# Kernel tuning notes

Hardware: AMD Instinct MI355X
Metric: run time of the kernel (lower is better)

Reference implementation:

```python
import math
import jax, jax.numpy as jnp
import numpy as np

B, S, E, H, P = 8, 1024, 512, 8, 32
MAXD, OFFS, LW, STL, HID = 256, 8.0, 4, 4, 2048

def _lin(x, w, b):
    return x @ w.T + b

def _gelu(x):
    return jax.nn.gelu(x, approximate=False)  # torch nn.GELU default (erf)

def _ln(x, g, b, eps=1e-5):
    m = x.mean(-1, keepdims=True)
    v = ((x - m) ** 2).mean(-1, keepdims=True)
    return (x - m) / jnp.sqrt(v + eps) * g + b

def setup_inputs() -> dict:
    key = jax.random.key(0)
    ks = iter(jax.random.split(key, 40))
    def w(*shape):
        return (jax.random.normal(next(ks), shape, dtype=jnp.float32) * 0.02)
    x = jax.random.normal(next(ks), (B, S, E), dtype=jnp.float32)
    lengths = jax.random.randint(next(ks), (B,), S // 2, S + 1)
    padding_mask = jnp.arange(S)[None, :] >= lengths[:, None]  # (B,S) bool
    inp = dict(x=x, padding_mask=padding_mask)
    # local MHA (torch nn.MultiheadAttention packed in_proj)
    inp.update(in_proj_w=w(3 * E, E), in_proj_b=jnp.zeros((3 * E,), jnp.float32),
               mha_out_w=w(E, E), mha_out_b=jnp.zeros((E,), jnp.float32))
    # deformable attention projections
    for nm in ('dq', 'dk', 'dv', 'do'):
        inp[nm + '_w'] = w(E, E); inp[nm + '_b'] = jnp.zeros((E,), jnp.float32)
    inp.update(off1_w=w(E, E), off1_b=jnp.zeros((E,), jnp.float32),
               off2_w=w(H * P, E), off2_b=jnp.zeros((H * P,), jnp.float32))
    inp.update(gate1_w=w(E, 3 * E), gate1_b=jnp.zeros((E,), jnp.float32),
               gate2_w=w(E, E), gate2_b=jnp.zeros((E,), jnp.float32))
    inp.update(n1_g=jnp.ones((E,), jnp.float32), n1_b=jnp.zeros((E,), jnp.float32),
               n2_g=jnp.ones((E,), jnp.float32), n2_b=jnp.zeros((E,), jnp.float32))
    inp.update(ffn1_w=w(HID, E), ffn1_b=jnp.zeros((HID,), jnp.float32),
               ffn2_w=w(E, HID), ffn2_b=jnp.zeros((E,), jnp.float32))
    return inp

def _forward(x, padding_mask, in_proj_w, in_proj_b, mha_out_w, mha_out_b,
             dq_w, dq_b, dk_w, dk_b, dv_w, dv_b, do_w, do_b,
             off1_w, off1_b, off2_w, off2_b, gate1_w, gate1_b, gate2_w, gate2_b,
             n1_g, n1_b, n2_g, n2_b, ffn1_w, ffn1_b, ffn2_w, ffn2_b):
    Bv, Sv, Ev = x.shape
    hd = Ev // H
    pos = jnp.arange(Sv)
    # ---------------- local causal windowed MHA ----------------
    qkv = _lin(x, in_proj_w, in_proj_b)
    q, k, v = jnp.split(qkv, 3, axis=-1)
    q = q.reshape(Bv, Sv, H, hd).transpose(0, 2, 1, 3)  # bhsd
    k = k.reshape(Bv, Sv, H, hd).transpose(0, 2, 1, 3)
    v = v.reshape(Bv, Sv, H, hd).transpose(0, 2, 1, 3)
    scores = jnp.einsum('bhqd,bhkd->bhqk', q, k) / math.sqrt(hd)
    future = pos[None, :] > pos[:, None]
    too_far = (pos[:, None] - pos[None, :]) >= min(LW, STL)
    lmask = (future | too_far)[None, None] | padding_mask[:, None, None, :]
    scores = jnp.where(lmask, -jnp.inf, scores)
    allm = lmask.all(-1, keepdims=True)
    scores = jnp.where(allm, 0.0, scores)  # avoid NaN on fully-masked (padded) rows
    attn = jax.nn.softmax(scores, axis=-1)
    attn = jnp.where(lmask, 0.0, attn)
    lo = jnp.einsum('bhqk,bhkd->bhqd', attn, v).transpose(0, 2, 1, 3).reshape(Bv, Sv, Ev)
    local_out = _lin(lo, mha_out_w, mha_out_b)
    # ---------------- deformable long-history attention ----------------
    anchors = jnp.linspace(0.1, 0.9, P)
    valid_len = jnp.clip(Sv - padding_mask.sum(-1), 1, None)
    positions = pos[None, :, None].astype(jnp.float32)  # (1,S,1)
    base = anchors[None, None, :] * positions
    off = jnp.tanh(_lin(_gelu(_lin(x, off1_w, off1_b)), off2_w, off2_b))
    off = off.reshape(Bv, Sv, H, P).mean(2) * OFFS
    sampled = base + off
    sampled = jnp.clip(sampled, jnp.clip(positions - MAXD, 0, None), positions)
    sampled = jnp.minimum(sampled, (valid_len - 1).astype(jnp.float32)[:, None, None])
    sp = jnp.round(sampled).astype(jnp.int32)  # (B,S,P) sample positions
    qd = _lin(x, dq_w, dq_b)
    kd = _lin(x, dk_w, dk_b)
    vd = _lin(x, dv_w, dv_b)
    bidx = jnp.arange(Bv)[:, None, None]
    k_sp = kd[bidx, sp]  # (B,S,P,E) gathered keys
    v_sp = vd[bidx, sp]
    sc = jnp.einsum('bqd,bqpd->bqp', qd, k_sp) / math.sqrt(Ev)
    samp_inv = padding_mask[bidx, sp]
    causal_inv = sp > pos[None, :, None]
    rb = jnp.clip(pos[:, None] - (STL - 1), 0, None)
    long_mem_mask = pos[None, :] >= rb  # (S,S): forbid recent short-term positions
    extra_inv = long_mem_mask[pos[None, :, None], sp]
    inv = samp_inv | causal_inv | extra_inv
    sc = jnp.where(inv, -jnp.inf, sc)
    alli = inv.all(-1, keepdims=True)
    sc = jnp.where(alli, 0.0, sc)
    a = jax.nn.softmax(sc, axis=-1)
    a = jnp.where(inv, 0.0, a)
    long_out = _lin(jnp.einsum('bqp,bqpd->bqd', a, v_sp), do_w, do_b)
    # ---------------- gate fuse + FFN ----------------
    cat = jnp.concatenate([x, local_out, long_out], axis=-1)
    g = jax.nn.sigmoid(_lin(_gelu(_lin(cat, gate1_w, gate1_b)), gate2_w, gate2_b))
    fused = g * local_out + (1.0 - g) * long_out
    x1 = _ln(x + fused, n1_g, n1_b)
    f = _lin(_gelu(_lin(x1, ffn1_w, ffn1_b)), ffn2_w, ffn2_b)
    return _ln(x1 + f, n2_g, n2_b)

def reference(x, padding_mask, in_proj_w, in_proj_b, mha_out_w, mha_out_b,
              dq_w, dq_b, dk_w, dk_b, dv_w, dv_b, do_w, do_b,
              off1_w, off1_b, off2_w, off2_b, gate1_w, gate1_b, gate2_w, gate2_b,
              n1_g, n1_b, n2_g, n2_b, ffn1_w, ffn1_b, ffn2_w, ffn2_b):
    return _forward(x, padding_mask, in_proj_w, in_proj_b, mha_out_w, mha_out_b,
                    dq_w, dq_b, dk_w, dk_b, dv_w, dv_b, do_w, do_b,
                    off1_w, off1_b, off2_w, off2_b, gate1_w, gate1_b, gate2_w, gate2_b,
                    n1_g, n1_b, n2_g, n2_b, ffn1_w, ffn1_b, ffn2_w, ffn2_b)
```

## Files before the change

### kernel.cpp

```cpp
#include <hip/hip_runtime.h>
#include <hip/hip_bf16.h>
#include <type_traits>

typedef __hip_bfloat16 bf16;
typedef __attribute__((ext_vector_type(8))) short short8;
typedef __attribute__((ext_vector_type(4))) float floatx4;

static constexpr int kB = 8;
static constexpr int kS = 1024;
static constexpr int kE = 512;
static constexpr int kH = 8;
static constexpr int kP = 32;
static constexpr int kTok = kB * kS;
static constexpr int kHid = 2048;

__device__ __forceinline__ void load8f(const bf16* p, float* f) {
  uint4 u = *(const uint4*)p;
  const bf16* h = (const bf16*)&u;
#pragma unroll
  for (int e = 0; e < 8; e++) f[e] = __bfloat162float(h[e]);
}
__device__ __forceinline__ void store8b(bf16* p, const float* f) {
  uint4 u;
  bf16* h = (bf16*)&u;
#pragma unroll
  for (int e = 0; e < 8; e++) h[e] = __float2bfloat16(f[e]);
  *(uint4*)p = u;
}
__device__ __forceinline__ bool is_pad(const void* pm, int flag, int idx) {
  return flag ? (((const int*)pm)[idx] != 0)
              : (((const unsigned char*)pm)[idx] != 0);
}
__device__ __forceinline__ float fast_gelu(float x) {
  float u = x * (0.7978845608f + 0.044714998f * x * x);
  float e = __expf(2.0f * u);
  float t = 1.0f - 2.0f / (e + 1.0f);
  return 0.5f * x * (1.0f + t);
}

__global__ __launch_bounds__(256) void detect_kernel(const void* __restrict__ x,
                                                     int* __restrict__ meta) {
  __shared__ int cnt;
  if (threadIdx.x == 0) cnt = 0;
  __syncthreads();
  const unsigned short* u = (const unsigned short*)x;
  int c = 0;
  for (int i = threadIdx.x; i < 1024; i += 256) {
    int e = (u[i] >> 7) & 0xFF;
    if (e >= 0x90) c++;
  }
  if (c) atomicAdd(&cnt, c);
  __syncthreads();
  if (threadIdx.x == 0) meta[9] = (cnt > 64) ? 1 : 0;
}

__global__ __launch_bounds__(256) void meta_kernel(const void* __restrict__ pm,
                                                   int* __restrict__ meta) {
  __shared__ int bigfound;
  __shared__ int cnt[kB];
  int tid = threadIdx.x;
  if (tid == 0) bigfound = 0;
  if (tid < kB) cnt[tid] = 0;
  __syncthreads();
  const unsigned int* w = (const unsigned int*)pm;
  int f = 0;
  for (int i = tid; i < 2048; i += 256)
    if (w[i] & 0xFFFFFFFEu) f = 1;
  if (f) atomicOr(&bigfound, 1);
  __syncthreads();
  int flag = bigfound ? 0 : 1;
  for (int i = tid; i < kTok; i += 256) {
    if (is_pad(pm, flag, i)) atomicAdd(&cnt[i >> 10], 1);
  }
  __syncthreads();
  if (tid == 0) meta[0] = flag;
  if (tid < kB) {
    int vl = kS - cnt[tid];
    if (vl < 1) vl = 1;
    meta[1 + tid] = vl;
  }
}

struct CvtJob { const void* src; bf16* hi; bf16* lo; int nblk; };
struct CvtJobs { CvtJob j[13]; };
__global__ __launch_bounds__(256) void cvt_all_kernel(CvtJobs jobs,
                                                      const int* __restrict__ meta) {
  int fp = meta[9];
  int b = blockIdx.x, ji = 0;
  while (b >= jobs.j[ji].nblk) { b -= jobs.j[ji].nblk; ji++; }
  CvtJob J = jobs.j[ji];
  int i = b * 1024 + threadIdx.x * 4;
  float v[4];
  if (fp) {
    float4 f = ((const float4*)J.src)[i >> 2];
    v[0] = f.x; v[1] = f.y; v[2] = f.z; v[3] = f.w;
  } else {
    uint2 u = *(const uint2*)((const bf16*)J.src + i);
    const bf16* h = (const bf16*)&u;
#pragma unroll
    for (int e = 0; e < 4; e++) v[e] = __bfloat162float(h[e]);
  }
  uint2 uh;
  bf16* hh = (bf16*)&uh;
#pragma unroll
  for (int e = 0; e < 4; e++) hh[e] = __float2bfloat16(v[e]);
  *(uint2*)(J.hi + i) = uh;
  if (J.lo) {
    uint2 ul;
    bf16* hl = (bf16*)&ul;
#pragma unroll
    for (int e = 0; e < 4; e++)
      hl[e] = __float2bfloat16(v[e] - __bfloat162float(hh[e]));
    *(uint2*)(J.lo + i) = ul;
  }
}

struct CvtFJob { const void* src; float* dst; int n; };
struct CvtFJobs { CvtFJob j[16]; };
__global__ __launch_bounds__(256) void cvt_small_kernel(CvtFJobs jobs,
                                                        const int* __restrict__ meta) {
  int fp = meta[9];
#pragma unroll 1
  for (int ji = 0; ji < 16; ji++) {
    CvtFJob J = jobs.j[ji];
    for (int i = threadIdx.x; i < J.n; i += 256)
      J.dst[i] = fp ? ((const float*)J.src)[i]
                    : __bfloat162float(((const bf16*)J.src)[i]);
  }
}

static constexpr int BK = 32, LDK = 40;

template <int BM, int BN, int ACT, typename OUTT>
__device__ __forceinline__ void gemm_core(const bf16* __restrict__ A,
                                          const bf16* __restrict__ W,
                                          const float* __restrict__ bias,
                                          OUTT* __restrict__ C, int N, int K,
                                          int m0, int n0) {
  constexpr int WR = (BM == 128 && BN == 128) ? 4 : 2;
  constexpr int WC = 4;
  __shared__ bf16 As[BM * LDK];
  __shared__ bf16 Bs[BN * LDK];
  const int tid = threadIdx.x;
  const int lane = tid & 63;
  const int wid = tid >> 6;
  int wm, wn;
  if constexpr (BM == 128 && BN == 128) {
    wm = (wid >> 1) * 64; wn = (wid & 1) * 64;
  } else {
    wm = wid * 32; wn = 0;
  }

  floatx4 acc[WR][WC];
#pragma unroll
  for (int i = 0; i < WR; i++)
#pragma unroll
    for (int j = 0; j < WC; j++) acc[i][j] = (floatx4)0.0f;

  for (int kt = 0; kt < K; kt += BK) {
#pragma unroll
    for (int c = 0; c < BM / 64; c++) {
      int v = c * 256 + tid;
      int row = v >> 2, off = (v & 3) * 8;
      *(uint4*)(&As[row * LDK + off]) =
          *(const uint4*)(&A[(size_t)(m0 + row) * K + kt + off]);
    }
#pragma unroll
    for (int c = 0; c < BN / 64; c++) {
      int v = c * 256 + tid;
      int row = v >> 2, off = (v & 3) * 8;
      *(uint4*)(&Bs[row * LDK + off]) =
          *(const uint4*)(&W[(size_t)(n0 + row) * K + kt + off]);
    }
    __syncthreads();
    const int ko = (lane >> 4) * 8;
    short8 af[WR], bfr[WC];
#pragma unroll
    for (int i = 0; i < WR; i++)
      af[i] = *(const short8*)(&As[(wm + i * 16 + (lane & 15)) * LDK + ko]);
#pragma unroll
    for (int j = 0; j < WC; j++)
      bfr[j] = *(const short8*)(&Bs[(wn + j * 16 + (lane & 15)) * LDK + ko]);
#pragma unroll
    for (int i = 0; i < WR; i++)
#pragma unroll
      for (int j = 0; j < WC; j++)
        acc[i][j] = __builtin_amdgcn_mfma_f32_16x16x32_bf16(bfr[j], af[i],
                                                            acc[i][j], 0, 0, 0);
    __syncthreads();
  }

#pragma unroll
  for (int i = 0; i < WR; i++) {
    int row = m0 + wm + i * 16 + (lane & 15);
#pragma unroll
    for (int j = 0; j < WC; j++) {
      int col = n0 + wn + j * 16 + ((lane >> 4) << 2);
      float bv[4] = {0.f, 0.f, 0.f, 0.f};
      if (bias) {
        float4 b4 = *(const float4*)&bias[col];
        bv[0] = b4.x; bv[1] = b4.y; bv[2] = b4.z; bv[3] = b4.w;
      }
      float v[4];
#pragma unroll
      for (int r = 0; r < 4; r++) {
        v[r] = acc[i][j][r] + bv[r];
        if (ACT == 1) v[r] = fast_gelu(v[r]);
        else if (ACT == 2) v[r] = 1.0f / (1.0f + __expf(-v[r]));
      }
      size_t idx = (size_t)row * N + col;
      if constexpr (std::is_same<OUTT, float>::value) {
        *(float4*)&C[idx] = make_float4(v[0], v[1], v[2], v[3]);
      } else {
        uint2 u;
        bf16* h = (bf16*)&u;
#pragma unroll
        for (int r = 0; r < 4; r++) h[r] = __float2bfloat16(v[r]);
        *(uint2*)&C[idx] = u;
      }
    }
  }
}

template <int BM, int BN, int ACT, typename OUTT>
__global__ __launch_bounds__(256) void gemm_bt(
    const bf16* __restrict__ A, const bf16* __restrict__ W,
    const float* __restrict__ bias, OUTT* __restrict__ C, int N, int K) {
  gemm_core<BM, BN, ACT, OUTT>(A, W, bias, C, N, K, blockIdx.x * BM,
                               blockIdx.y * BN);
}

__global__ __launch_bounds__(256) void gemm_pair(
    const bf16* __restrict__ A0, const bf16* __restrict__ W0,
    const float* __restrict__ b0, bf16* __restrict__ C0,
    const bf16* __restrict__ A1, const bf16* __restrict__ W1,
    const float* __restrict__ b1, bf16* __restrict__ C1, int N, int K) {
  int nb = N >> 6;
  bool s = (int)blockIdx.y >= nb;
  gemm_core<128, 64, 0, bf16>(s ? A1 : A0, s ? W1 : W0, s ? b1 : b0,
                              s ? C1 : C0, N, K, blockIdx.x * 128,
                              (s ? (int)blockIdx.y - nb : (int)blockIdx.y) * 64);
}

__global__ __launch_bounds__(256) void gemm_gate1(
    const bf16* __restrict__ x, const bf16* __restrict__ lo,
    const bf16* __restrict__ lg, const bf16* __restrict__ W,
    const float* __restrict__ bias, bf16* __restrict__ C) {
  constexpr int BM = 128, BN = 64, WR = 2, WC = 4;
  constexpr int N = 512, K = 1536;
  __shared__ bf16 As[BM * LDK];
  __shared__ bf16 Bs[BN * LDK];
  const int tid = threadIdx.x;
  const int lane = tid & 63;
  const int wid = tid >> 6;
  const int wm = wid * 32, wn = 0;
  const int m0 = blockIdx.x * BM, n0 = blockIdx.y * BN;

  floatx4 acc[WR][WC];
#pragma unroll
  for (int i = 0; i < WR; i++)
#pragma unroll
    for (int j = 0; j < WC; j++) acc[i][j] = (floatx4)0.0f;

  for (int kt = 0; kt < K; kt += BK) {
#pragma unroll
    for (int c = 0; c < 2; c++) {
      int v = c * 256 + tid;
      int row = v >> 2, off = (v & 3) * 8;
      int k = kt + off;
      const bf16* src = (k < 512) ? x : (k < 1024) ? lo : lg;
      int kk = k & 511;
      *(uint4*)(&As[row * LDK + off]) =
          *(const uint4*)(&src[(size_t)(m0 + row) * 512 + kk]);
    }
    {
      int v = tid;
      int row = v >> 2, off = (v & 3) * 8;
      *(uint4*)(&Bs[row * LDK + off]) =
          *(const uint4*)(&W[(size_t)(n0 + row) * K + kt + off]);
    }
    __syncthreads();
    const int ko = (lane >> 4) * 8;
    short8 af[WR], bfr[WC];
#pragma unroll
    for (int i = 0; i < WR; i++)
      af[i] = *(const short8*)(&As[(wm + i * 16 + (lane & 15)) * LDK + ko]);
#pragma unroll
    for (int j = 0; j < WC; j++)
      bfr[j] = *(const short8*)(&Bs[(wn + j * 16 + (lane & 15)) * LDK + ko]);
#pragma unroll
    for (int i = 0; i < WR; i++)
#pragma unroll
      for (int j = 0; j < WC; j++)
        acc[i][j] = __builtin_amdgcn_mfma_f32_16x16x32_bf16(bfr[j], af[i],
                                                            acc[i][j], 0, 0, 0);
    __syncthreads();
  }

#pragma unroll
  for (int i = 0; i < WR; i++) {
    int row = m0 + wm + i * 16 + (lane & 15);
#pragma unroll
    for (int j = 0; j < WC; j++) {
      int col = n0 + wn + j * 16 + ((lane >> 4) << 2);
      float4 b4 = *(const float4*)&bias[col];
      float bv[4] = {b4.x, b4.y, b4.z, b4.w};
      uint2 u;
      bf16* h = (bf16*)&u;
#pragma unroll
      for (int r = 0; r < 4; r++)
        h[r] = __float2bfloat16(fast_gelu(acc[i][j][r] + bv[r]));
      *(uint2*)&C[(size_t)row * N + col] = u;
    }
  }
}

template <int BM, int BN>
__global__ __launch_bounds__(256) void gemm3_bt(
    const bf16* __restrict__ Ah, const bf16* __restrict__ Al,
    const bf16* __restrict__ Wh, const bf16* __restrict__ Wl,
    const float* __restrict__ bias, float* __restrict__ C, int N, int K) {
  constexpr int WR = 2;
  constexpr int WC = (BM == 128) ? 4 : 2;
  __shared__ bf16 Ash[BM * LDK];
  __shared__ bf16 Asl[BM * LDK];
  __shared__ bf16 Bsh[BN * LDK];
  __shared__ bf16 Bsl[BN * LDK];
  const int tid = threadIdx.x;
  const int lane = tid & 63;
  const int wid = tid >> 6;
  int wm, wn;
  if constexpr (BM == 128) {
    wm = wid * 32; wn = 0;
  } else {
    wm = (wid >> 1) * 32; wn = (wid & 1) * 32;
  }
  const int m0 = blockIdx.x * BM, n0 = blockIdx.y * BN;

  floatx4 acc[WR][WC];
#pragma unroll
  for (int i = 0; i < WR; i++)
#pragma unroll
    for (int j = 0; j < WC; j++) acc[i][j] = (floatx4)0.0f;

  for (int kt = 0; kt < K; kt += BK) {
#pragma unroll
    for (int c = 0; c < BM / 64; c++) {
      int v = c * 256 + tid;
      int row = v >> 2, off = (v & 3) * 8;
      size_t g = (size_t)(m0 + row) * K + kt + off;
      *(uint4*)(&Ash[row * LDK + off]) = *(const uint4*)(&Ah[g]);
      *(uint4*)(&Asl[row * LDK + off]) = *(const uint4*)(&Al[g]);
    }
#pragma unroll
    for (int c = 0; c < BN / 64; c++) {
      int v = c * 256 + tid;
      int row = v >> 2, off = (v & 3) * 8;
      size_t g = (size_t)(n0 + row) * K + kt + off;
      *(uint4*)(&Bsh[row * LDK + off]) = *(const uint4*)(&Wh[g]);
      *(uint4*)(&Bsl[row * LDK + off]) = *(const uint4*)(&Wl[g]);
    }
    __syncthreads();
    const int ko = (lane >> 4) * 8;
    short8 ah[WR], al[WR], bh[WC], bl[WC];
#pragma unroll
    for (int i = 0; i < WR; i++) {
      int ro = (wm + i * 16 + (lane & 15)) * LDK + ko;
      ah[i] = *(const short8*)(&Ash[ro]);
      al[i] = *(const short8*)(&Asl[ro]);
    }
#pragma unroll
    for (int j = 0; j < WC; j++) {
      int ro = (wn + j * 16 + (lane & 15)) * LDK + ko;
      bh[j] = *(const short8*)(&Bsh[ro]);
      bl[j] = *(const short8*)(&Bsl[ro]);
    }
#pragma unroll
    for (int i = 0; i < WR; i++)
#pragma unroll
      for (int j = 0; j < WC; j++) {
        acc[i][j] = __builtin_amdgcn_mfma_f32_16x16x32_bf16(bh[j], ah[i],
                                                            acc[i][j], 0, 0, 0);
        acc[i][j] = __builtin_amdgcn_mfma_f32_16x16x32_bf16(bl[j], ah[i],
                                                            acc[i][j], 0, 0, 0);
        acc[i][j] = __builtin_amdgcn_mfma_f32_16x16x32_bf16(bh[j], al[i],
                                                            acc[i][j], 0, 0, 0);
      }
    __syncthreads();
  }

#pragma unroll
  for (int i = 0; i < WR; i++) {
    int row = m0 + wm + i * 16 + (lane & 15);
#pragma unroll
    for (int j = 0; j < WC; j++) {
      int col = n0 + wn + j * 16 + ((lane >> 4) << 2);
      float4 b4 = *(const float4*)&bias[col];
      float bv[4] = {b4.x, b4.y, b4.z, b4.w};
      float v[4];
#pragma unroll
      for (int r = 0; r < 4; r++) v[r] = acc[i][j][r] + bv[r];
      *(float4*)&C[(size_t)row * N + col] = make_float4(v[0], v[1], v[2], v[3]);
    }
  }
}

__global__ __launch_bounds__(256) void local_attn_kernel(
    const bf16* __restrict__ qkv, const void* __restrict__ pm,
    const int* __restrict__ meta, bf16* __restrict__ lo) {
  int lane = threadIdx.x & 63;
  int t = blockIdx.x * 4 + (threadIdx.x >> 6);
  int b = t >> 10, s = t & 1023;
  int h = lane >> 3, sub = lane & 7;
  int flag = meta[0];
  float q[8];
  load8f(qkv + (size_t)t * 3072 + h * 64 + sub * 8, q);
  float sc[4];
  bool val[4];
#pragma unroll
  for (int w = 0; w < 4; w++) {
    int kp = s - 3 + w;
    bool v = (kp >= 0) && !is_pad(pm, flag, b * kS + kp);
    float d = 0.0f;
    if (v) {
      float kk[8];
      load8f(qkv + (size_t)(b * kS + kp) * 3072 + 512 + h * 64 + sub * 8, kk);
#pragma unroll
      for (int e = 0; e < 8; e++) d += q[e] * kk[e];
    }
    d += __shfl_xor(d, 1);
    d += __shfl_xor(d, 2);
    d += __shfl_xor(d, 4);
    sc[w] = v ? d / 8.0f : -INFINITY;
    val[w] = v;
  }
  float mx = fmaxf(fmaxf(sc[0], sc[1]), fmaxf(sc[2], sc[3]));
  float a[4] = {0.f, 0.f, 0.f, 0.f};
  if (mx != -INFINITY) {
    float ssum = 0.f;
#pragma unroll
    for (int w = 0; w < 4; w++) {
      float e = val[w] ? expf(sc[w] - mx) : 0.0f;
      a[w] = e;
      ssum += e;
    }
#pragma unroll
    for (int w = 0; w < 4; w++) a[w] /= ssum;
  }
  float o[8] = {0.f, 0.f, 0.f, 0.f, 0.f, 0.f, 0.f, 0.f};
#pragma unroll
  for (int w = 0; w < 4; w++) {
    if (val[w] && a[w] > 0.0f) {
      int kp = s - 3 + w;
      float vv[8];
      load8f(qkv + (size_t)(b * kS + kp) * 3072 + 1024 + h * 64 + sub * 8, vv);
#pragma unroll
      for (int e = 0; e < 8; e++) o[e] += a[w] * vv[e];
    }
  }
  store8b(lo + (size_t)t * kE + lane * 8, o);
}

__global__ __launch_bounds__(256) void gelu_split_kernel(
    const float* __restrict__ S, bf16* __restrict__ hi, bf16* __restrict__ lo) {
  int i = (blockIdx.x * 256 + threadIdx.x) * 4;
#pragma unroll
  for (int c = 0; c < 4; c++) {
    float v = S[i + c];
    float g = 0.5f * v * (1.0f + erff(v * 0.70710678118654752f));
    bf16 a = __float2bfloat16(g);
    hi[i + c] = a;
    lo[i + c] = __float2bfloat16(g - __bfloat162float(a));
  }
}

__global__ __launch_bounds__(256) void sampler_kernel(
    const float* __restrict__ rawf, const void* __restrict__ pm,
    const int* __restrict__ meta, int* __restrict__ sp,
    unsigned int* __restrict__ invm) {
  int t = blockIdx.x * 8 + (threadIdx.x >> 5);
  int p = threadIdx.x & 31;
  int b = t >> 10, s = t & 1023;
  int flag = meta[0];
  float off = 0.0f;
#pragma unroll
  for (int h = 0; h < kH; h++) off += tanhf(rawf[(size_t)t * 256 + h * kP + p]);
  double anchor = 0.1 + 0.8 * (double)p / 31.0;
  double sampled = anchor * (double)s + (double)off;
  double lov = fmax(0.0, (double)s - 256.0);
  sampled = fmin(fmax(sampled, lov), (double)s);
  int vlen = meta[1 + b];
  sampled = fmin(sampled, (double)(vlen - 1));
  int spv = (int)rint(sampled);
  bool inv = is_pad(pm, flag, b * kS + spv) || (spv > s) ||
             (spv >= max(0, s - 3));
  sp[(size_t)t * kP + p] = spv;
  unsigned long long m = __ballot(inv);
  int lane = threadIdx.x & 63;
  if (lane == 0) invm[t] = (unsigned int)m;
  if (lane == 32) invm[t] = (unsigned int)(m >> 32);
}

__global__ __launch_bounds__(256) void long_attn_kernel(
    const bf16* __restrict__ qkv, const int* __restrict__ sp,
    const unsigned int* __restrict__ invm, bf16* __restrict__ ctx) {
  int lane = threadIdx.x & 63;
  int bid = blockIdx.x;
  int sbid = (bid & 7) * 256 + (bid >> 3);
  int t = sbid * 4 + (threadIdx.x >> 6);
  int b = t >> 10;
  int p = lane & 31;
  int row_abs = b * kS + sp[(size_t)t * kP + p];
  float q[8];
  load8f(qkv + (size_t)t * 3072 + 1536 + lane * 8, q);
  float sc_mine = 0.0f;
#pragma unroll 4
  for (int pp = 0; pp < 32; pp++) {
    int row = __shfl(row_abs, pp);
    float kk[8];
    load8f(qkv + (size_t)row * 3072 + 2048 + lane * 8, kk);
    float d = 0.0f;
#pragma unroll
    for (int e = 0; e < 8; e++) d += q[e] * kk[e];
#pragma unroll
    for (int m = 1; m < 64; m <<= 1) d += __shfl_xor(d, m);
    if (p == pp) sc_mine = d;
  }
  bool inv = (invm[t] >> p) & 1u;
  float sc = inv ? -INFINITY : sc_mine / 22.627416997969522f;
  float mx = sc;
#pragma unroll
  for (int m = 1; m < 32; m <<= 1) mx = fmaxf(mx, __shfl_xor(mx, m));
  float e = (inv || mx == -INFINITY) ? 0.0f : expf(sc - mx);
  float ssum = e;
#pragma unroll
  for (int m = 1; m < 32; m <<= 1) ssum += __shfl_xor(ssum, m);
  float a = (ssum > 0.0f) ? e / ssum : 0.0f;
  float o[8] = {0.f, 0.f, 0.f, 0.f, 0.f, 0.f, 0.f, 0.f};
#pragma unroll 4
  for (int pp = 0; pp < 32; pp++) {
    float ap = __shfl(a, pp);
    int row = __shfl(row_abs, pp);
    if (ap != 0.0f) {
      float vv[8];
      load8f(qkv + (size_t)row * 3072 + 2560 + lane * 8, vv);
#pragma unroll
      for (int e2 = 0; e2 < 8; e2++) o[e2] += ap * vv[e2];
    }
  }
  store8b(ctx + (size_t)t * kE + lane * 8, o);
}

__global__ __launch_bounds__(256) void ln1_kernel(
    const void* __restrict__ xin, const int* __restrict__ meta,
    const bf16* __restrict__ lo, const bf16* __restrict__ lg,
    const bf16* __restrict__ g, const float* __restrict__ gamma,
    const float* __restrict__ beta, bf16* __restrict__ x1b,
    float* __restrict__ x1f) {
  int lane = threadIdx.x & 63;
  int t = blockIdx.x * 4 + (threadIdx.x >> 6);
  size_t base = (size_t)t * kE + lane * 8;
  float xv[8], lov[8], lgv[8], gv[8], h[8];
  if (meta[9]) {
    const float4* xf = (const float4*)((const float*)xin + base);
    float4 a = xf[0], b2 = xf[1];
    xv[0] = a.x; xv[1] = a.y; xv[2] = a.z; xv[3] = a.w;
    xv[4] = b2.x; xv[5] = b2.y; xv[6] = b2.z; xv[7] = b2.w;
  } else {
    load8f((const bf16*)xin + base, xv);
  }
  load8f(lo + base, lov);
  load8f(lg + base, lgv);
  load8f(g + base, gv);
  float s1 = 0.f, s2 = 0.f;
#pragma unroll
  for (int e = 0; e < 8; e++) {
    h[e] = xv[e] + gv[e] * lov[e] + (1.0f - gv[e]) * lgv[e];
    s1 += h[e];
    s2 += h[e] * h[e];
  }
#pragma unroll
  for (int m = 1; m < 64; m <<= 1) {
    s1 += __shfl_xor(s1, m);
    s2 += __shfl_xor(s2, m);
  }
  float mean = s1 * (1.0f / kE);
  float var = s2 * (1.0f / kE) - mean * mean;
  float rstd = 1.0f / sqrtf(var + 1e-5f);
  float y[8];
#pragma unroll
  for (int e = 0; e < 8; e++)
    y[e] = (h[e] - mean) * rstd * gamma[lane * 8 + e] + beta[lane * 8 + e];
  store8b(x1b + base, y);
#pragma unroll
  for (int e = 0; e < 8; e++) x1f[base + e] = y[e];
}

__global__ __launch_bounds__(256) void ln2_kernel(
    const float* __restrict__ x1f, const float* __restrict__ ff,
    const float* __restrict__ gamma, const float* __restrict__ beta,
    const int* __restrict__ meta, void* __restrict__ out) {
  int lane = threadIdx.x & 63;
  int t = blockIdx.x * 4 + (threadIdx.x >> 6);
  size_t base = (size_t)t * kE + lane * 8;
  float h[8];
  float s1 = 0.f, s2 = 0.f;
#pragma unroll
  for (int e = 0; e < 8; e++) {
    h[e] = x1f[base + e] + ff[base + e];
    s1 += h[e];
    s2 += h[e] * h[e];
  }
#pragma unroll
  for (int m = 1; m < 64; m <<= 1) {
    s1 += __shfl_xor(s1, m);
    s2 += __shfl_xor(s2, m);
  }
  float mean = s1 * (1.0f / kE);
  float var = s2 * (1.0f / kE) - mean * mean;
  float rstd = 1.0f / sqrtf(var + 1e-5f);
  float y[8];
#pragma unroll
  for (int e = 0; e < 8; e++)
    y[e] = (h[e] - mean) * rstd * gamma[lane * 8 + e] + beta[lane * 8 + e];
  if (meta[9]) {
    float* of = (float*)out + base;
    ((float4*)of)[0] = make_float4(y[0], y[1], y[2], y[3]);
    ((float4*)of)[1] = make_float4(y[4], y[5], y[6], y[7]);
  } else {
    store8b((bf16*)out + base, y);
  }
}

extern "C" void kernel_launch(void* const* d_in, const int* in_sizes, int n_in,
                              void* d_out, int out_size, void* d_ws,
                              size_t ws_size, hipStream_t stream) {
  const void* x = d_in[0];
  const void* pm = d_in[1];

  char* w = (char*)d_ws;
  auto alloc = [&](size_t bytes) {
    char* p = w;
    w += (bytes + 255) & ~(size_t)255;
    return p;
  };
  bf16* qkv_all = (bf16*)alloc((size_t)kTok * 3072 * 2);
  bf16* lo_ctx = (bf16*)alloc((size_t)kTok * kE * 2);
  bf16* ctx2 = (bf16*)alloc((size_t)kTok * kE * 2);
  bf16* local_out = (bf16*)alloc((size_t)kTok * kE * 2);
  bf16* long_out = (bf16*)alloc((size_t)kTok * kE * 2);
  bf16* hbuf = (bf16*)alloc((size_t)kTok * kE * 2);
  bf16* gbuf = (bf16*)alloc((size_t)kTok * kE * 2);
  bf16* x1b = (bf16*)alloc((size_t)kTok * kE * 2);
  float* x1f = (float*)alloc((size_t)kTok * kE * 4);
  float* rawf = (float*)alloc((size_t)kTok * 256 * 4);
  int* sp = (int*)alloc((size_t)kTok * kP * 4);
  unsigned int* invm = (unsigned int*)alloc((size_t)kTok * 4);
  int* meta = (int*)alloc(256);
  bf16* x_hi = (bf16*)alloc((size_t)kTok * kE * 2);
  bf16* x_lo = (bf16*)alloc((size_t)kTok * kE * 2);
  bf16* wall = (bf16*)alloc((size_t)3072 * 512 * 2);
  bf16* mow = (bf16*)alloc(512 * 512 * 2);
  bf16* dow = (bf16*)alloc(512 * 512 * 2);
  bf16* o1h = (bf16*)alloc(512 * 512 * 2);
  bf16* o1l = (bf16*)alloc(512 * 512 * 2);
  bf16* o2h = (bf16*)alloc(256 * 512 * 2);
  bf16* o2l = (bf16*)alloc(256 * 512 * 2);
  bf16* g1w = (bf16*)alloc(512 * 1536 * 2);
  bf16* g2w = (bf16*)alloc(512 * 512 * 2);
  bf16* f1w = (bf16*)alloc((size_t)2048 * 512 * 2);
  bf16* f2w = (bf16*)alloc((size_t)512 * 2048 * 2);
  float* ball = (float*)alloc(3072 * 4);
  float* mob = (float*)alloc(512 * 4);
  float* dob = (float*)alloc(512 * 4);
  float* o1b = (float*)alloc(512 * 4);
  float* o2b = (float*)alloc(256 * 4);
  float* g1b = (float*)alloc(512 * 4);
  float* g2b = (float*)alloc(512 * 4);
  float* n1g = (float*)alloc(512 * 4);
  float* n1bt = (float*)alloc(512 * 4);
  float* n2g = (float*)alloc(512 * 4);
  float* n2bt = (float*)alloc(512 * 4);
  float* f1b = (float*)alloc(2048 * 4);
  float* f2b = (float*)alloc(512 * 4);

  float* S32 = x1f;
  bf16* h_hi = hbuf;
  bf16* h_lo = x1b;
  float* f_f32 = (float*)qkv_all;
  bf16* ffn_h = (bf16*)((char*)qkv_all + (size_t)kTok * kE * 4);

  dim3 blk(256);
  detect_kernel<<<1, blk, 0, stream>>>(x, meta);
  meta_kernel<<<1, blk, 0, stream>>>(pm, meta);

  CvtJobs J;
  auto job = [](const void* s, bf16* hi, bf16* lo, int n) {
    CvtJob j; j.src = s; j.hi = hi; j.lo = lo; j.nblk = n >> 10; return j;
  };
  J.j[0] = job(d_in[0], x_hi, x_lo, kTok * kE);
  J.j[1] = job(d_in[2], wall, nullptr, 1536 * 512);
  J.j[2] = job(d_in[6], wall + (size_t)1536 * 512, nullptr, 512 * 512);
  J.j[3] = job(d_in[8], wall + (size_t)2048 * 512, nullptr, 512 * 512);
  J.j[4] = job(d_in[10], wall + (size_t)2560 * 512, nullptr, 512 * 512);
  J.j[5] = job(d_in[4], mow, nullptr, 512 * 512);
  J.j[6] = job(d_in[12], dow, nullptr, 512 * 512);
  J.j[7] = job(d_in[14], o1h, o1l, 512 * 512);
  J.j[8] = job(d_in[16], o2h, o2l, 256 * 512);
  J.j[9] = job(d_in[18], g1w, nullptr, 512 * 1536);
  J.j[10] = job(d_in[20], g2w, nullptr, 512 * 512);
  J.j[11] = job(d_in[26], f1w, nullptr, 2048 * 512);
  J.j[12] = job(d_in[28], f2w, nullptr, 512 * 2048);
  int totblk = 0;
  for (int i = 0; i < 13; i++) totblk += J.j[i].nblk;
  cvt_all_kernel<<<totblk, blk, 0, stream>>>(J, meta);

  CvtFJobs JF;
  auto fjob = [](const void* s, float* d, int n) {
    CvtFJob j; j.src = s; j.dst = d; j.n = n; return j;
  };
  JF.j[0] = fjob(d_in[3], ball, 1536);
  JF.j[1] = fjob(d_in[7], ball + 1536, 512);
  JF.j[2] = fjob(d_in[9], ball + 2048, 512);
  JF.j[3] = fjob(d_in[11], ball + 2560, 512);
  JF.j[4] = fjob(d_in[5], mob, 512);
  JF.j[5] = fjob(d_in[13], dob, 512);
  JF.j[6] = fjob(d_in[15], o1b, 512);
  JF.j[7] = fjob(d_in[17], o2b, 256);
  JF.j[8] = fjob(d_in[19], g1b, 512);
  JF.j[9] = fjob(d_in[21], g2b, 512);
  JF.j[10] = fjob(d_in[22], n1g, 512);
  JF.j[11] = fjob(d_in[23], n1bt, 512);
  JF.j[12] = fjob(d_in[24], n2g, 512);
  JF.j[13] = fjob(d_in[25], n2bt, 512);
  JF.j[14] = fjob(d_in[27], f1b, 2048);
  JF.j[15] = fjob(d_in[29], f2b, 512);
  cvt_small_kernel<<<1, blk, 0, stream>>>(JF, meta);

  gemm_bt<128, 128, 0, bf16><<<dim3(64, 24), blk, 0, stream>>>(
      x_hi, wall, ball, qkv_all, 3072, kE);
  gemm3_bt<128, 64><<<dim3(64, 8), blk, 0, stream>>>(
      x_hi, x_lo, o1h, o1l, o1b, S32, kE, kE);
  local_attn_kernel<<<2048, blk, 0, stream>>>(qkv_all, pm, meta, lo_ctx);
  gelu_split_kernel<<<4096, blk, 0, stream>>>(S32, h_hi, h_lo);
  gemm3_bt<64, 64><<<dim3(128, 4), blk, 0, stream>>>(
      h_hi, h_lo, o2h, o2l, o2b, rawf, 256, kE);
  sampler_kernel<<<1024, blk, 0, stream>>>(rawf, pm, meta, sp, invm);
  long_attn_kernel<<<2048, blk, 0, stream>>>(qkv_all, sp, invm, ctx2);

  gemm_pair<<<dim3(64, 16), blk, 0, stream>>>(lo_ctx, mow, mob, local_out,
                                              ctx2, dow, dob, long_out, kE, kE);

  gemm_gate1<<<dim3(64, 8), blk, 0, stream>>>(x_hi, local_out, long_out, g1w,
                                              g1b, hbuf);
  gemm_bt<128, 64, 2, bf16><<<dim3(64, 8), blk, 0, stream>>>(
      hbuf, g2w, g2b, gbuf, kE, kE);

  ln1_kernel<<<2048, blk, 0, stream>>>(x, meta, local_out, long_out, gbuf, n1g,
                                       n1bt, x1b, x1f);
  gemm_bt<128, 128, 1, bf16><<<dim3(64, 16), blk, 0, stream>>>(
      x1b, f1w, f1b, ffn_h, kHid, kE);
  gemm_bt<128, 64, 0, float><<<dim3(64, 8), blk, 0, stream>>>(
      ffn_h, f2w, f2b, f_f32, kE, kHid);
  ln2_kernel<<<2048, blk, 0, stream>>>(x1f, f_f32, n2g, n2bt, meta, d_out);
}
```

Before: 489.8 us.

## Use direct global-to-LDS loads with XOR swizzle and fuse GELU split into GEMM

All GEMM kernels now stage their A/B tiles with global_load_lds DMA into unpadded shared memory. An XOR swizzle replaces the padding to avoid bank conflicts, and this removes the register round-trip for tile loads. Separately, the GELU plus hi/lo bf16 split moves into the epilogue of the first offset GEMM, which removes one kernel launch and an fp32 intermediate write and read. The swizzle and lane-to-row mapping must match the DMA's wave-contiguous write pattern exactly, or results will be wrong.

```diff
diff --git a/kernel.cpp b/kernel.cpp
--- a/kernel.cpp
+++ b/kernel.cpp
@@ -36,6 +36,11 @@
   float e = __expf(2.0f * u);
   float t = 1.0f - 2.0f / (e + 1.0f);
   return 0.5f * x * (1.0f + t);
+}
+__device__ __forceinline__ void dma16(const bf16* g, bf16* l) {
+  __builtin_amdgcn_global_load_lds(
+      (const __attribute__((address_space(1))) unsigned int*)g,
+      (__attribute__((address_space(3))) unsigned int*)l, 16, 0, 0);
 }
 
 __global__ __launch_bounds__(256) void detect_kernel(const void* __restrict__ x,
@@ -129,7 +134,7 @@
   }
 }
 
-static constexpr int BK = 32, LDK = 40;
+static constexpr int BK = 32;
 
 template <int BM, int BN, int ACT, typename OUTT>
 __device__ __forceinline__ void gemm_core(const bf16* __restrict__ A,
@@ -139,8 +144,8 @@
                                           int m0, int n0) {
   constexpr int WR = (BM == 128 && BN == 128) ? 4 : 2;
   constexpr int WC = 4;
-  __shared__ bf16 As[BM * LDK];
-  __shared__ bf16 Bs[BN * LDK];
+  __shared__ bf16 As[BM * BK];
+  __shared__ bf16 Bs[BN * BK];
   const int tid = threadIdx.x;
   const int lane = tid & 63;
   const int wid = tid >> 6;
@@ -160,27 +165,31 @@
   for (int kt = 0; kt < K; kt += BK) {
 #pragma unroll
     for (int c = 0; c < BM / 64; c++) {
-      int v = c * 256 + tid;
-      int row = v >> 2, off = (v & 3) * 8;
-      *(uint4*)(&As[row * LDK + off]) =
-          *(const uint4*)(&A[(size_t)(m0 + row) * K + kt + off]);
+      int seg = c * 64 + wid * 16;
+      int row = seg + (lane >> 2);
+      int ch = (lane & 3) ^ ((row >> 1) & 3);
+      dma16(&A[(size_t)(m0 + row) * K + kt + ch * 8], &As[seg * BK]);
     }
 #pragma unroll
     for (int c = 0; c < BN / 64; c++) {
-      int v = c * 256 + tid;
-      int row = v >> 2, off = (v & 3) * 8;
-      *(uint4*)(&Bs[row * LDK + off]) =
-          *(const uint4*)(&W[(size_t)(n0 + row) * K + kt + off]);
+      int seg = c * 64 + wid * 16;
+      int row = seg + (lane >> 2);
+      int ch = (lane & 3) ^ ((row >> 1) & 3);
+      dma16(&W[(size_t)(n0 + row) * K + kt + ch * 8], &Bs[seg * BK]);
     }
     __syncthreads();
-    const int ko = (lane >> 4) * 8;
+    const int kb = lane >> 4;
     short8 af[WR], bfr[WC];
 #pragma unroll
-    for (int i = 0; i < WR; i++)
-      af[i] = *(const short8*)(&As[(wm + i * 16 + (lane & 15)) * LDK + ko]);
-#pragma unroll
-    for (int j = 0; j < WC; j++)
-      bfr[j] = *(const short8*)(&Bs[(wn + j * 16 + (lane & 15)) * LDK + ko]);
+    for (int i = 0; i < WR; i++) {
+      int r = wm + i * 16 + (lane & 15);
+      af[i] = *(const short8*)(&As[r * BK + ((kb ^ ((r >> 1) & 3)) << 3)]);
+    }
+#pragma unroll
+    for (int j = 0; j < WC; j++) {
+      int r = wn + j * 16 + (lane & 15);
+      bfr[j] = *(const short8*)(&Bs[r * BK + ((kb ^ ((r >> 1) & 3)) << 3)]);
+    }
 #pragma unroll
     for (int i = 0; i < WR; i++)
 #pragma unroll
@@ -248,8 +257,8 @@
     const float* __restrict__ bias, bf16* __restrict__ C) {
   constexpr int BM = 128, BN = 64, WR = 2, WC = 4;
   constexpr int N = 512, K = 1536;
-  __shared__ bf16 As[BM * LDK];
-  __shared__ bf16 Bs[BN * LDK];
+  __shared__ bf16 As[BM * BK];
+  __shared__ bf16 Bs[BN * BK];
   const int tid = threadIdx.x;
   const int lane = tid & 63;
   const int wid = tid >> 6;
@@ -263,31 +272,34 @@
     for (int j = 0; j < WC; j++) acc[i][j] = (floatx4)0.0f;
 
   for (int kt = 0; kt < K; kt += BK) {
+    const bf16* src = (kt < 512) ? x : (kt < 1024) ? lo : lg;
+    int kk = kt & 511;
 #pragma unroll
     for (int c = 0; c < 2; c++) {
-      int v = c * 256 + tid;
-      int row = v >> 2, off = (v & 3) * 8;
-      int k = kt + off;
-      const bf16* src = (k < 512) ? x : (k < 1024) ? lo : lg;
-      int kk = k & 511;
-      *(uint4*)(&As[row * LDK + off]) =
-          *(const uint4*)(&src[(size_t)(m0 + row) * 512 + kk]);
+      int seg = c * 64 + wid * 16;
+      int row = seg + (lane >> 2);
+      int ch = (lane & 3) ^ ((row >> 1) & 3);
+      dma16(&src[(size_t)(m0 + row) * 512 + kk + ch * 8], &As[seg * BK]);
     }
     {
-      int v = tid;
-      int row = v >> 2, off = (v & 3) * 8;
-      *(uint4*)(&Bs[row * LDK + off]) =
-          *(const uint4*)(&W[(size_t)(n0 + row) * K + kt + off]);
+      int seg = wid * 16;
+      int row = seg + (lane >> 2);
+      int ch = (lane & 3) ^ ((row >> 1) & 3);
+      dma16(&W[(size_t)(n0 + row) * K + kt + ch * 8], &Bs[seg * BK]);
     }
     __syncthreads();
-    const int ko = (lane >> 4) * 8;
+    const int kb = lane >> 4;
     short8 af[WR], bfr[WC];
 #pragma unroll
-    for (int i = 0; i < WR; i++)
-      af[i] = *(const short8*)(&As[(wm + i * 16 + (lane & 15)) * LDK + ko]);
-#pragma unroll
-    for (int j = 0; j < WC; j++)
-      bfr[j] = *(const short8*)(&Bs[(wn + j * 16 + (lane & 15)) * LDK + ko]);
+    for (int i = 0; i < WR; i++) {
+      int r = wm + i * 16 + (lane & 15);
+      af[i] = *(const short8*)(&As[r * BK + ((kb ^ ((r >> 1) & 3)) << 3)]);
+    }
+#pragma unroll
+    for (int j = 0; j < WC; j++) {
+      int r = wn + j * 16 + (lane & 15);
+      bfr[j] = *(const short8*)(&Bs[r * BK + ((kb ^ ((r >> 1) & 3)) << 3)]);
+    }
 #pragma unroll
     for (int i = 0; i < WR; i++)
 #pragma unroll
@@ -315,17 +327,18 @@
   }
 }
 
-template <int BM, int BN>
+template <int BM, int BN, bool SPLIT>
 __global__ __launch_bounds__(256) void gemm3_bt(
     const bf16* __restrict__ Ah, const bf16* __restrict__ Al,
     const bf16* __restrict__ Wh, const bf16* __restrict__ Wl,
-    const float* __restrict__ bias, float* __restrict__ C, int N, int K) {
+    const float* __restrict__ bias, float* __restrict__ Cf,
+    bf16* __restrict__ Chi, bf16* __restrict__ Clo, int N, int K) {
   constexpr int WR = 2;
   constexpr int WC = (BM == 128) ? 4 : 2;
-  __shared__ bf16 Ash[BM * LDK];
-  __shared__ bf16 Asl[BM * LDK];
-  __shared__ bf16 Bsh[BN * LDK];
-  __shared__ bf16 Bsl[BN * LDK];
+  __shared__ bf16 Ash[BM * BK];
+  __shared__ bf16 Asl[BM * BK];
+  __shared__ bf16 Bsh[BN * BK];
+  __shared__ bf16 Bsl[BN * BK];
   const int tid = threadIdx.x;
   const int lane = tid & 63;
   const int wid = tid >> 6;
@@ -346,32 +359,36 @@
   for (int kt = 0; kt < K; kt += BK) {
 #pragma unroll
     for (int c = 0; c < BM / 64; c++) {
-      int v = c * 256 + tid;
-      int row = v >> 2, off = (v & 3) * 8;
-      size_t g = (size_t)(m0 + row) * K + kt + off;
-      *(uint4*)(&Ash[row * LDK + off]) = *(const uint4*)(&Ah[g]);
-      *(uint4*)(&Asl[row * LDK + off]) = *(const uint4*)(&Al[g]);
+      int seg = c * 64 + wid * 16;
+      int row = seg + (lane >> 2);
+      int ch = (lane & 3) ^ ((row >> 1) & 3);
+      size_t g = (size_t)(m0 + row) * K + kt + ch * 8;
+      dma16(&Ah[g], &Ash[seg * BK]);
+      dma16(&Al[g], &Asl[seg * BK]);
     }
 #pragma unroll
     for (int c = 0; c < BN / 64; c++) {
-      int v = c * 256 + tid;
-      int row = v >> 2, off = (v & 3) * 8;
-      size_t g = (size_t)(n0 + row) * K + kt + off;
-      *(uint4*)(&Bsh[row * LDK + off]) = *(const uint4*)(&Wh[g]);
-      *(uint4*)(&Bsl[row * LDK + off]) = *(const uint4*)(&Wl[g]);
+      int seg = c * 64 + wid * 16;
+      int row = seg + (lane >> 2);
+      int ch = (lane & 3) ^ ((row >> 1) & 3);
+      size_t g = (size_t)(n0 + row) * K + kt + ch * 8;
+      dma16(&Wh[g], &Bsh[seg * BK]);
+      dma16(&Wl[g], &Bsl[seg * BK]);
     }
     __syncthreads();
-    const int ko = (lane >> 4) * 8;
+    const int kb = lane >> 4;
     short8 ah[WR], al[WR], bh[WC], bl[WC];
 #pragma unroll
     for (int i = 0; i < WR; i++) {
-      int ro = (wm + i * 16 + (lane & 15)) * LDK + ko;
+      int r = wm + i * 16 + (lane & 15);
+      int ro = r * BK + ((kb ^ ((r >> 1) & 3)) << 3);
       ah[i] = *(const short8*)(&Ash[ro]);
       al[i] = *(const short8*)(&Asl[ro]);
     }
 #pragma unroll
     for (int j = 0; j < WC; j++) {
-      int ro = (wn + j * 16 + (lane & 15)) * LDK + ko;
+      int r = wn + j * 16 + (lane & 15);
+      int ro = r * BK + ((kb ^ ((r >> 1) & 3)) << 3);
       bh[j] = *(const short8*)(&Bsh[ro]);
       bl[j] = *(const short8*)(&Bsl[ro]);
     }
@@ -397,10 +414,25 @@
       int col = n0 + wn + j * 16 + ((lane >> 4) << 2);
       float4 b4 = *(const float4*)&bias[col];
       float bv[4] = {b4.x, b4.y, b4.z, b4.w};
-      float v[4];
-#pragma unroll
-      for (int r = 0; r < 4; r++) v[r] = acc[i][j][r] + bv[r];
-      *(float4*)&C[(size_t)row * N + col] = make_float4(v[0], v[1], v[2], v[3]);
+      if constexpr (SPLIT) {
+        uint2 uh, ul;
+        bf16* hh = (bf16*)&uh;
+        bf16* hl = (bf16*)&ul;
+#pragma unroll
+        for (int r = 0; r < 4; r++) {
+          float v = acc[i][j][r] + bv[r];
+          float g = 0.5f * v * (1.0f + erff(v * 0.70710678118654752f));
+          bf16 hi = __float2bfloat16(g);
+          hh[r] = hi;
+          hl[r] = __float2bfloat16(g - __bfloat162float(hi));
+        }
+        *(uint2*)&Chi[(size_t)row * N + col] = uh;
+        *(uint2*)&Clo[(size_t)row * N + col] = ul;
+      } else {
+        *(float4*)&Cf[(size_t)row * N + col] =
+            make_float4(acc[i][j][0] + bv[0], acc[i][j][1] + bv[1],
+                        acc[i][j][2] + bv[2], acc[i][j][3] + bv[3]);
+      }
     }
   }
 }
@@ -459,19 +491,6 @@
     }
   }
   store8b(lo + (size_t)t * kE + lane * 8, o);
-}
-
-__global__ __launch_bounds__(256) void gelu_split_kernel(
-    const float* __restrict__ S, bf16* __restrict__ hi, bf16* __restrict__ lo) {
-  int i = (blockIdx.x * 256 + threadIdx.x) * 4;
-#pragma unroll
-  for (int c = 0; c < 4; c++) {
-    float v = S[i + c];
-    float g = 0.5f * v * (1.0f + erff(v * 0.70710678118654752f));
-    bf16 a = __float2bfloat16(g);
-    hi[i + c] = a;
-    lo[i + c] = __float2bfloat16(g - __bfloat162float(a));
-  }
 }
 
 __global__ __launch_bounds__(256) void sampler_kernel(
@@ -684,7 +703,6 @@
   float* f1b = (float*)alloc(2048 * 4);
   float* f2b = (float*)alloc(512 * 4);
 
-  float* S32 = x1f;
   bf16* h_hi = hbuf;
   bf16* h_lo = x1b;
   float* f_f32 = (float*)qkv_all;
@@ -739,12 +757,11 @@
 
   gemm_bt<128, 128, 0, bf16><<<dim3(64, 24), blk, 0, stream>>>(
       x_hi, wall, ball, qkv_all, 3072, kE);
-  gemm3_bt<128, 64><<<dim3(64, 8), blk, 0, stream>>>(
-      x_hi, x_lo, o1h, o1l, o1b, S32, kE, kE);
+  gemm3_bt<128, 64, true><<<dim3(64, 8), blk, 0, stream>>>(
+      x_hi, x_lo, o1h, o1l, o1b, nullptr, h_hi, h_lo, kE, kE);
   local_attn_kernel<<<2048, blk, 0, stream>>>(qkv_all, pm, meta, lo_ctx);
-  gelu_split_kernel<<<4096, blk, 0, stream>>>(S32, h_hi, h_lo);
-  gemm3_bt<64, 64><<<dim3(128, 4), blk, 0, stream>>>(
-      h_hi, h_lo, o2h, o2l, o2b, rawf, 256, kE);
+  gemm3_bt<64, 64, false><<<dim3(128, 4), blk, 0, stream>>>(
+      h_hi, h_lo, o2h, o2l, o2b, rawf, nullptr, nullptr, 256, kE);
   sampler_kernel<<<1024, blk, 0, stream>>>(rawf, pm, meta, sp, invm);
   long_attn_kernel<<<2048, blk, 0, stream>>>(qkv_all, sp, invm, ctx2);
 
```

Result: faster. 477.1 us (-2.6%).
